# Optimization experiments

Hardware: AMD Instinct MI355X
Metric: run time of the kernel (lower is better)

Reference implementation:

```python
import jax, jax.numpy as jnp
import numpy as np

CHEB_K = 3

def avwgcn(x, E, W_pool, b_pool):
    # x: [B,N,Cin], E: [N,e], W_pool: [e,K,Cin,Cout], b_pool: [e,Cout]
    N = E.shape[0]
    A = jax.nn.softmax(jax.nn.relu(E @ E.T), axis=1)          # adaptive adjacency [N,N]
    supports = [jnp.eye(N, dtype=x.dtype), A]
    for _ in range(2, CHEB_K):
        supports.append(2.0 * (A @ supports[-1]) - supports[-2])
    S = jnp.stack(supports)                                    # [K,N,N]
    W = jnp.einsum('ne,ekio->nkio', E, W_pool)                 # per-node weights
    b = E @ b_pool                                             # [N,Cout]
    xg = jnp.einsum('knm,bmi->bnki', S, x)                     # Chebyshev graph conv
    return jnp.einsum('bnki,nkio->bno', xg, W) + b


def setup_inputs() -> dict:
    key = jax.random.key(0)
    ks = jax.random.split(key, 7)
    B, N, Din, Dout, E_DIM = 64, 1024, 64, 64, 16
    C = Din + Dout
    return {
        'x': jax.random.normal(ks[0], (B, N, Din), dtype=jnp.float32),
        'state': jax.random.normal(ks[1], (B, N, Dout), dtype=jnp.float32),
        'node_embeddings': jax.random.normal(ks[2], (N, E_DIM), dtype=jnp.float32),
        'gate_W_pool': jax.random.normal(ks[3], (E_DIM, CHEB_K, C, 2 * Dout), dtype=jnp.float32) * 0.1,
        'gate_b_pool': jax.random.normal(ks[4], (E_DIM, 2 * Dout), dtype=jnp.float32) * 0.1,
        'upd_W_pool': jax.random.normal(ks[5], (E_DIM, CHEB_K, C, Dout), dtype=jnp.float32) * 0.1,
        'upd_b_pool': jax.random.normal(ks[6], (E_DIM, Dout), dtype=jnp.float32) * 0.1,
    }


def reference(x, state, node_embeddings, gate_W_pool, gate_b_pool, upd_W_pool, upd_b_pool):
    hidden_dim = state.shape[-1]
    input_and_state = jnp.concatenate([x, state], axis=-1)
    z_r = jax.nn.sigmoid(avwgcn(input_and_state, node_embeddings, gate_W_pool, gate_b_pool))
    z, r = z_r[..., :hidden_dim], z_r[..., hidden_dim:]
    candidate = jnp.concatenate([x, z * state], axis=-1)
    hc = jnp.tanh(avwgcn(candidate, node_embeddings, upd_W_pool, upd_b_pool))
    return r * state + (1.0 - r) * hc
```

## Files before the change

kernel.cpp:

```cpp
#include <hip/hip_runtime.h>
#include <math.h>

#define N_NODES 1024
#define B_SZ 64
#define GNH 4096
#define KI 384
#define EDIM 16
#define WG_NODE 49152
#define WG_WAVE 12288
#define WU_NODE 24576
#define WU_WAVE 6144

typedef _Float16 half8_t __attribute__((ext_vector_type(8)));
typedef float f32x4 __attribute__((ext_vector_type(4)));

__device__ __forceinline__ unsigned short f2h(float f) {
    _Float16 h = (_Float16)f;
    return *(unsigned short*)&h;
}
__device__ __forceinline__ float h2f(unsigned short u) {
    _Float16 h = *(_Float16*)&u;
    return (float)h;
}
__device__ __forceinline__ float sigmoidf_(float v) {
    return 1.f / (1.f + __expf(-v));
}
__device__ __forceinline__ void load_lds16(const void* g, void* l) {
    __builtin_amdgcn_global_load_lds(
        (const __attribute__((address_space(1))) void*)g,
        (__attribute__((address_space(3))) void*)l, 16, 0, 0);
}

__global__ __launch_bounds__(256) void compute_A_kernel(
    const float* __restrict__ E, unsigned short* __restrict__ Ah) {
    __shared__ float red[256];
    const int tid = threadIdx.x;
    const int n = blockIdx.x;
    float en[EDIM];
#pragma unroll
    for (int e = 0; e < EDIM; ++e) en[e] = E[n * EDIM + e];
    float logit[4], lmax = -1e30f;
#pragma unroll
    for (int j = 0; j < 4; ++j) {
        const int m = tid + j * 256;
        float d = 0.f;
#pragma unroll
        for (int e = 0; e < EDIM; ++e) d += en[e] * E[m * EDIM + e];
        d = fmaxf(d, 0.f);
        logit[j] = d;
        lmax = fmaxf(lmax, d);
    }
    red[tid] = lmax;
    __syncthreads();
    for (int s = 128; s > 0; s >>= 1) {
        if (tid < s) red[tid] = fmaxf(red[tid], red[tid + s]);
        __syncthreads();
    }
    lmax = red[0];
    __syncthreads();
    float ex[4], lsum = 0.f;
#pragma unroll
    for (int j = 0; j < 4; ++j) {
        ex[j] = __expf(logit[j] - lmax);
        lsum += ex[j];
    }
    red[tid] = lsum;
    __syncthreads();
    for (int s = 128; s > 0; s >>= 1) {
        if (tid < s) red[tid] += red[tid + s];
        __syncthreads();
    }
    const float inv = 1.f / red[0];
#pragma unroll
    for (int j = 0; j < 4; ++j)
        Ah[n * N_NODES + tid + j * 256] = f2h(ex[j] * inv);
}

__global__ __launch_bounds__(256) void build_T0_all_kernel(
    const float* __restrict__ x, const float* __restrict__ state,
    unsigned short* __restrict__ TX0, unsigned short* __restrict__ TS0,
    unsigned short* __restrict__ TX0T, unsigned short* __restrict__ TS0T) {
    __shared__ unsigned short Lx[64 * 72];
    __shared__ unsigned short Lss[64 * 72];
    const int tid = threadIdx.x;
    const int n0 = blockIdx.x * 64;
    const int b = blockIdx.y;
#pragma unroll
    for (int t = 0; t < 16; ++t) {
        const int id = t * 256 + tid;
        const int nl = id >> 6;
        const int c = id & 63;
        const float xv = x[((size_t)b * N_NODES + n0 + nl) * 64 + c];
        const float sv = state[((size_t)b * N_NODES + n0 + nl) * 64 + c];
        const unsigned short xh = f2h(xv), sh = f2h(sv);
        TX0[(size_t)(n0 + nl) * GNH + b * 64 + c] = xh;
        TS0[(size_t)(n0 + nl) * GNH + b * 64 + c] = sh;
        Lx[c * 72 + nl] = xh;
        Lss[c * 72 + nl] = sh;
    }
    __syncthreads();
#pragma unroll
    for (int t = 0; t < 2; ++t) {
        const int id = t * 256 + tid;
        const int c = id >> 3;
        const int n8 = id & 7;
        uint4 xv = *(const uint4*)&Lx[c * 72 + n8 * 8];
        uint4 sv = *(const uint4*)&Lss[c * 72 + n8 * 8];
        *(uint4*)&TX0T[(size_t)(b * 64 + c) * N_NODES + n0 + n8 * 8] = xv;
        *(uint4*)&TS0T[(size_t)(b * 64 + c) * N_NODES + n0 + n8 * 8] = sv;
    }
}

__global__ __launch_bounds__(256) void transpose16_kernel(
    const unsigned short* __restrict__ src, unsigned short* __restrict__ dst,
    int W) {
    __shared__ unsigned short Ls[64 * 72];
    const int tid = threadIdx.x;
    const int r0 = blockIdx.x * 64;
    const int c0 = blockIdx.y * 64;
#pragma unroll
    for (int t = 0; t < 2; ++t) {
        const int id = t * 256 + tid;
        const int row = id >> 3;
        const int c8 = id & 7;
        uint4 v = *(const uint4*)&src[(size_t)(r0 + row) * W + c0 + c8 * 8];
        const unsigned short* vp = (const unsigned short*)&v;
#pragma unroll
        for (int j = 0; j < 8; ++j) Ls[(c8 * 8 + j) * 72 + row] = vp[j];
    }
    __syncthreads();
#pragma unroll
    for (int t = 0; t < 2; ++t) {
        const int id = t * 256 + tid;
        const int c = id >> 3;
        const int r8 = id & 7;
        uint4 v = *(const uint4*)&Ls[c * 72 + r8 * 8];
        *(uint4*)&dst[(size_t)(c0 + c) * N_NODES + r0 + r8 * 8] = v;
    }
}

__global__ __launch_bounds__(256) void gemm_s2_kernel(
    const unsigned short* __restrict__ Ah,
    const unsigned short* __restrict__ AhT, unsigned short* __restrict__ S2h) {
    __shared__ unsigned short As[64 * 64];
    __shared__ unsigned short Bs[64 * 64];
    const int tid = threadIdx.x;
    const int wave = tid >> 6;
    const int lane = tid & 63;
    const int l15 = lane & 15;
    const int quad = lane >> 4;
    const int n0 = blockIdx.x * 64;
    const int m0 = blockIdx.y * 64;
    const int wn = wave * 16;
    const int lr = lane >> 3;
    const int lsw = (lane & 7) ^ lr;

    f32x4 acc[4] = {};
    for (int k0 = 0; k0 < N_NODES; k0 += 64) {
#pragma unroll
        for (int i = 0; i < 2; ++i) {
            const int rbase = (wave * 2 + i) * 8;
            load_lds16(&Ah[(size_t)(n0 + rbase + lr) * N_NODES + k0 + lsw * 8],
                       &As[rbase * 64]);
            load_lds16(&AhT[(size_t)(m0 + rbase + lr) * N_NODES + k0 + lsw * 8],
                       &Bs[rbase * 64]);
        }
        __syncthreads();
#pragma unroll
        for (int ks = 0; ks < 2; ++ks) {
            const int slot = ((ks * 4 + quad) ^ (l15 & 7)) * 8;
            const half8_t b = *(const half8_t*)&Bs[(wn + l15) * 64 + slot];
#pragma unroll
            for (int mi = 0; mi < 4; ++mi) {
                const half8_t a = *(const half8_t*)&As[(mi * 16 + l15) * 64 + slot];
                acc[mi] =
                    __builtin_amdgcn_mfma_f32_16x16x32_f16(a, b, acc[mi], 0, 0, 0);
            }
        }
        __syncthreads();
    }
#pragma unroll
    for (int mi = 0; mi < 4; ++mi) {
#pragma unroll
        for (int r = 0; r < 4; ++r) {
            const int n_g = n0 + mi * 16 + quad * 4 + r;
            const int m_g = m0 + wn + l15;
            const float v = 2.f * acc[mi][r] - (n_g == m_g ? 1.f : 0.f);
            S2h[(size_t)n_g * N_NODES + m_g] = f2h(v);
        }
    }
}

template <int BM>
__global__ __launch_bounds__(512, 2) void gemm_graph8_kernel(
    const unsigned short* __restrict__ Ah,
    const unsigned short* __restrict__ S2h,
    const unsigned short* __restrict__ BTX,
    const unsigned short* __restrict__ BTS,
    unsigned short* __restrict__ T1X, unsigned short* __restrict__ T1S,
    unsigned short* __restrict__ T2X, unsigned short* __restrict__ T2S,
    int ysplit, int colsPerXcd) {
    constexpr int MFR = BM / 32;
    constexpr int ASLOT_H = BM * 32;
    constexpr int SLOT_H = ASLOT_H + 8192;
    constexpr int APASS = BM / 128;
    constexpr int MT = 2048 / BM;
    __shared__ unsigned short lds[4 * SLOT_H];

    const int tid = threadIdx.x;
    const int wave = tid >> 6;
    const int lane = tid & 63;
    const int l15 = lane & 15;
    const int quad = lane >> 4;
    const int wm = (wave >> 2) * (BM / 2);
    const int wn = (wave & 3) * 64;

    const int id = blockIdx.x;
    const int xcd = id & 7;
    const int j = id >> 3;
    const int mtile = j & (MT - 1);
    const int ytile = xcd * colsPerXcd + j / MT;
    const int mrow0 = mtile * BM;
    const bool isA = mrow0 < N_NODES;
    const unsigned short* Asrc =
        (isA ? Ah : S2h) + (size_t)(mrow0 & 1023) * N_NODES;
    const bool isX = ytile < ysplit;
    const int col0 = (isX ? ytile : ytile - ysplit) * 256;
    const unsigned short* Bsrc = (isX ? BTX : BTS) + (size_t)col0 * N_NODES;
    unsigned short* OUT = (isA ? (isX ? T1X : T1S) : (isX ? T2X : T2S)) +
                          (size_t)(mrow0 & 1023) * GNH + col0;

    int goff[2];
#pragma unroll
    for (int jp = 0; jp < 2; ++jp) {
        const int cell = jp * 512 + tid;
        const int prow = cell >> 3;
        const int q = (cell & 7) ^ (prow & 7);
        goff[jp] = (2 * prow + (q >> 2)) * N_NODES + (q & 3) * 8;
    }

    int offA[MFR], offB[4];
#pragma unroll
    for (int mi = 0; mi < MFR; ++mi) {
        const int prow = (wm >> 1) + mi * 8 + (l15 >> 1);
        const int s8 = ((l15 & 1) * 4 + quad) ^ (prow & 7);
        offA[mi] = prow * 64 + s8 * 8;
    }
#pragma unroll
    for (int ni = 0; ni < 4; ++ni) {
        const int pcol = (wn >> 1) + ni * 8 + (l15 >> 1);
        const int s8 = ((l15 & 1) * 4 + quad) ^ (pcol & 7);
        offB[ni] = ASLOT_H + pcol * 64 + s8 * 8;
    }

    f32x4 acc[MFR][4] = {};

    auto stageA = [&](int t) {
        const int sl = t & 3;
#pragma unroll
        for (int jp = 0; jp < APASS; ++jp)
            load_lds16(Asrc + (size_t)t * 32 + goff[jp],
                       &lds[sl * SLOT_H + jp * 4096 + wave * 512]);
    };
    auto stageB = [&](int t) {
        const int sl = t & 3;
#pragma unroll
        for (int jp = 0; jp < 2; ++jp)
            load_lds16(Bsrc + (size_t)t * 32 + goff[jp],
                       &lds[sl * SLOT_H + ASLOT_H + jp * 4096 + wave * 512]);
    };
    auto waitPipe = [&] {
        if constexpr (BM == 256)
            asm volatile("s_waitcnt vmcnt(8)" ::: "memory");
        else
            asm volatile("s_waitcnt vmcnt(6)" ::: "memory");
    };

    auto tileBody = [&](int t, bool tail) {
        const unsigned short* base = &lds[(t & 3) * SLOT_H];
        half8_t a[MFR], b[4];
#pragma unroll
        for (int mi = 0; mi < MFR; ++mi)
            a[mi] = *(const half8_t*)&base[offA[mi]];
#pragma unroll
        for (int ni = 0; ni < 4; ++ni)
            b[ni] = *(const half8_t*)&base[offB[ni]];
        if (!tail) {
            stageA(t + 3);
            stageB(t + 3);
        }
        __builtin_amdgcn_sched_barrier(0);
        asm volatile("s_waitcnt lgkmcnt(0)" ::: "memory");
        __builtin_amdgcn_sched_barrier(0);
        __builtin_amdgcn_s_setprio(1);
#pragma unroll
        for (int mi = 0; mi < MFR; ++mi)
#pragma unroll
            for (int ni = 0; ni < 4; ++ni)
                acc[mi][ni] = __builtin_amdgcn_mfma_f32_16x16x32_f16(
                    a[mi], b[ni], acc[mi][ni], 0, 0, 0);
        __builtin_amdgcn_s_setprio(0);
        __builtin_amdgcn_sched_barrier(0);
        if (!tail) {
            waitPipe();
        } else {
            asm volatile("s_waitcnt vmcnt(0)" ::: "memory");
        }
        __builtin_amdgcn_sched_barrier(0);
        __builtin_amdgcn_s_barrier();
    };

    stageA(0); stageB(0);
    stageA(1); stageB(1);
    stageA(2); stageB(2);
    waitPipe();
    __builtin_amdgcn_s_barrier();
    __builtin_amdgcn_sched_barrier(0);

#pragma unroll 4
    for (int t = 0; t < 28; ++t) tileBody(t, false);
    tileBody(28, false);
    tileBody(29, true);
    tileBody(30, true);
    tileBody(31, true);

    constexpr int NPASS = BM / 64;
#pragma unroll
    for (int p = 0; p < NPASS; ++p) {
        __syncthreads();
        const int whalf = (BM == 256) ? (p >> 1) : p;
        const int mi0 = (BM == 256) ? (p & 1) * 4 : 0;
        if ((wave >> 2) == whalf) {
#pragma unroll
            for (int mi = 0; mi < 4; ++mi)
#pragma unroll
                for (int ni = 0; ni < 4; ++ni)
#pragma unroll
                    for (int r = 0; r < 4; ++r) {
                        const int row = mi * 16 + quad * 4 + r;
                        const int col = wn + ni * 16 + l15;
                        lds[row * 264 + col] = f2h(acc[mi0 + mi][ni][r]);
                    }
        }
        __syncthreads();
#pragma unroll
        for (int i = 0; i < 4; ++i) {
            const int id2 = i * 512 + tid;
            const int row = id2 >> 5;
            const int c8 = id2 & 31;
            uint4 v = *(const uint4*)&lds[row * 264 + c8 * 8];
            *(uint4*)&OUT[(size_t)(p * 64 + row) * GNH + c8 * 8] = v;
        }
    }
}

__global__ __launch_bounds__(256) void dequant_gate_kernel(
    const float* __restrict__ Wp, const float* __restrict__ E,
    unsigned short* __restrict__ Wt) {
    __shared__ float En[32 * 16];
    const int tid = threadIdx.x;
    const int c8 = blockIdx.x * 256 + tid;
    const int n0 = blockIdx.y * 32;
    const int sub = c8 & 1;
    const int c = c8 >> 1;
    const int l15 = c & 15;
    const int quad = (c >> 4) & 3;
    const int half = (c >> 6) & 1;
    const int ks = (c >> 7) & 3;
    const int sq = c >> 9;
    const int s = sq % 3;
    const int w = sq / 3;
    const int k0 = s * 128 + (ks * 4 + quad) * 8 + sub * 4;
    const int o = w * 32 + half * 16 + l15;

#pragma unroll
    for (int t = 0; t < 2; ++t) {
        const int id = t * 256 + tid;
        En[id] = E[(n0 + (id >> 4)) * EDIM + (id & 15)];
    }
    __syncthreads();

    f32x4 wv[EDIM];
#pragma unroll
    for (int e = 0; e < EDIM; ++e) {
        f32x4 v;
#pragma unroll
        for (int j = 0; j < 4; ++j)
            v[j] = Wp[(size_t)(e * KI + k0 + j) * 128 + o];
        wv[e] = v;
    }

#pragma unroll 4
    for (int nl = 0; nl < 32; ++nl) {
        f32x4 a = {0.f, 0.f, 0.f, 0.f};
#pragma unroll
        for (int e = 0; e < EDIM; ++e) a += wv[e] * En[nl * EDIM + e];
        union { unsigned short u[4]; uint2 v; } pk;
#pragma unroll
        for (int j = 0; j < 4; ++j) pk.u[j] = f2h(a[j]);
        *(uint2*)&Wt[(size_t)(n0 + nl) * WG_NODE + (size_t)c8 * 4] = pk.v;
    }
}

__global__ __launch_bounds__(256) void dequant_upd_kernel(
    const float* __restrict__ Wp, const float* __restrict__ E,
    unsigned short* __restrict__ Wt) {
    __shared__ float En[32 * 16];
    const int tid = threadIdx.x;
    const int c8 = blockIdx.x * 256 + tid;
    const int n0 = blockIdx.y * 32;
    const int sub = c8 & 1;
    const int c = c8 >> 1;
    const int l15 = c & 15;
    const int quad = (c >> 4) & 3;
    const int ks = (c >> 6) & 3;
    const int sq = c >> 8;
    const int s = sq % 3;
    const int w = sq / 3;
    const int k0 = s * 128 + (ks * 4 + quad) * 8 + sub * 4;
    const int o = w * 16 + l15;

#pragma unroll
    for (int t = 0; t < 2; ++t) {
        const int id = t * 256 + tid;
        En[id] = E[(n0 + (id >> 4)) * EDIM + (id & 15)];
    }
    __syncthreads();

    f32x4 wv[EDIM];
#pragma unroll
    for (int e = 0; e < EDIM; ++e) {
        f32x4 v;
#pragma unroll
        for (int j = 0; j < 4; ++j)
            v[j] = Wp[(size_t)(e * KI + k0 + j) * 64 + o];
        wv[e] = v;
    }

#pragma unroll 4
    for (int nl = 0; nl < 32; ++nl) {
        f32x4 a = {0.f, 0.f, 0.f, 0.f};
#pragma unroll
        for (int e = 0; e < EDIM; ++e) a += wv[e] * En[nl * EDIM + e];
        union { unsigned short u[4]; uint2 v; } pk;
#pragma unroll
        for (int j = 0; j < 4; ++j) pk.u[j] = f2h(a[j]);
        *(uint2*)&Wt[(size_t)(n0 + nl) * WU_NODE + (size_t)c8 * 4] = pk.v;
    }
}

__global__ __launch_bounds__(256) void pernode_gate_kernel(
    const unsigned short* __restrict__ TX0,
    const unsigned short* __restrict__ TS0,
    const unsigned short* __restrict__ TX1,
    const unsigned short* __restrict__ TS1,
    const unsigned short* __restrict__ TX2,
    const unsigned short* __restrict__ TS2,
    const unsigned short* __restrict__ Wt, const float* __restrict__ E,
    const float* __restrict__ bp, const float* __restrict__ state,
    unsigned short* __restrict__ rbuf, unsigned short* __restrict__ cand) {
    __shared__ unsigned short XsX[64 * 64];
    __shared__ unsigned short XsS[64 * 64];
    const int n = blockIdx.x;
    const int tid = threadIdx.x;
    const int wave = tid >> 6;
    const int lane = tid & 63;
    const int l15 = lane & 15;
    const int quad = lane >> 4;
    const int wn = wave * 32;
    const int lr = lane >> 3;
    const int lsw = (lane & 7) ^ lr;

    float bias[2];
#pragma unroll
    for (int ni = 0; ni < 2; ++ni) {
        float bv = 0.f;
#pragma unroll
        for (int e = 0; e < EDIM; ++e)
            bv += E[n * EDIM + e] * bp[e * 128 + wn + ni * 16 + l15];
        bias[ni] = bv;
    }

    f32x4 acc[4][2] = {};

    const unsigned short* TXs[3] = {TX0, TX1, TX2};
    const unsigned short* TSs[3] = {TS0, TS1, TS2};
    const unsigned short* wbase =
        Wt + ((size_t)n * 4 + wave) * WG_WAVE + lane * 8;

    for (int s = 0; s < 3; ++s) {
        const unsigned short* xs = TXs[s] + (size_t)n * GNH;
        const unsigned short* ss = TSs[s] + (size_t)n * GNH;
#pragma unroll
        for (int i = 0; i < 2; ++i) {
            const int slab = wave * 2 + i;
            load_lds16(xs + (slab * 8 + lr) * 64 + lsw * 8, &XsX[slab * 512]);
            load_lds16(ss + (slab * 8 + lr) * 64 + lsw * 8, &XsS[slab * 512]);
        }
        __syncthreads();
#pragma unroll
        for (int ks = 0; ks < 4; ++ks) {
            const int kseg = ks * 4 + quad;
            half8_t b[2];
            b[0] = *(const half8_t*)&wbase[((s * 4 + ks) * 2 + 0) * 512];
            b[1] = *(const half8_t*)&wbase[((s * 4 + ks) * 2 + 1) * 512];
            const unsigned short* plane = (kseg < 8) ? XsX : XsS;
            const int aslot = ((kseg & 7) ^ (l15 & 7)) * 8;
#pragma unroll
            for (int mi = 0; mi < 4; ++mi) {
                const half8_t a =
                    *(const half8_t*)&plane[(mi * 16 + l15) * 64 + aslot];
#pragma unroll
                for (int ni = 0; ni < 2; ++ni)
                    acc[mi][ni] = __builtin_amdgcn_mfma_f32_16x16x32_f16(
                        a, b[ni], acc[mi][ni], 0, 0, 0);
            }
        }
        __syncthreads();
    }

#pragma unroll
    for (int mi = 0; mi < 4; ++mi) {
#pragma unroll
        for (int r = 0; r < 4; ++r) {
            const int b_g = mi * 16 + quad * 4 + r;
#pragma unroll
            for (int ni = 0; ni < 2; ++ni) {
                const int o_g = wn + ni * 16 + l15;
                const float v = sigmoidf_(acc[mi][ni][r] + bias[ni]);
                if (o_g < 64) {
                    const float sv =
                        state[((size_t)b_g * N_NODES + n) * 64 + o_g];
                    cand[(size_t)n * GNH + b_g * 64 + o_g] = f2h(v * sv);
                } else {
                    rbuf[((size_t)n * B_SZ + b_g) * 64 + (o_g - 64)] = f2h(v);
                }
            }
        }
    }
}

__global__ __launch_bounds__(256) void pernode_upd_kernel(
    const unsigned short* __restrict__ TX0,
    const unsigned short* __restrict__ CAND,
    const unsigned short* __restrict__ TX1,
    const unsigned short* __restrict__ TS1,
    const unsigned short* __restrict__ TX2,
    const unsigned short* __restrict__ TS2,
    const unsigned short* __restrict__ Wt, const float* __restrict__ E,
    const float* __restrict__ bp, const float* __restrict__ state,
    const unsigned short* __restrict__ rbuf, float* __restrict__ out) {
    __shared__ unsigned short XsX[64 * 64];
    __shared__ unsigned short XsS[64 * 64];
    const int n = blockIdx.x;
    const int tid = threadIdx.x;
    const int wave = tid >> 6;
    const int lane = tid & 63;
    const int l15 = lane & 15;
    const int quad = lane >> 4;
    const int wn = wave * 16;
    const int o_g = wn + l15;
    const int lr = lane >> 3;
    const int lsw = (lane & 7) ^ lr;

    float bias = 0.f;
#pragma unroll
    for (int e = 0; e < EDIM; ++e)
        bias += E[n * EDIM + e] * bp[e * 64 + o_g];

    f32x4 acc[4] = {};

    const unsigned short* TXs[3] = {TX0, TX1, TX2};
    const unsigned short* TSs[3] = {CAND, TS1, TS2};
    const unsigned short* wbase =
        Wt + ((size_t)n * 4 + wave) * WU_WAVE + lane * 8;

    for (int s = 0; s < 3; ++s) {
        const unsigned short* xs = TXs[s] + (size_t)n * GNH;
        const unsigned short* ss = TSs[s] + (size_t)n * GNH;
#pragma unroll
        for (int i = 0; i < 2; ++i) {
            const int slab = wave * 2 + i;
            load_lds16(xs + (slab * 8 + lr) * 64 + lsw * 8, &XsX[slab * 512]);
            load_lds16(ss + (slab * 8 + lr) * 64 + lsw * 8, &XsS[slab * 512]);
        }
        __syncthreads();
#pragma unroll
        for (int ks = 0; ks < 4; ++ks) {
            const int kseg = ks * 4 + quad;
            const half8_t b = *(const half8_t*)&wbase[(s * 4 + ks) * 512];
            const unsigned short* plane = (kseg < 8) ? XsX : XsS;
            const int aslot = ((kseg & 7) ^ (l15 & 7)) * 8;
#pragma unroll
            for (int mi = 0; mi < 4; ++mi) {
                const half8_t a =
                    *(const half8_t*)&plane[(mi * 16 + l15) * 64 + aslot];
                acc[mi] = __builtin_amdgcn_mfma_f32_16x16x32_f16(a, b, acc[mi],
                                                                 0, 0, 0);
            }
        }
        __syncthreads();
    }

#pragma unroll
    for (int mi = 0; mi < 4; ++mi) {
#pragma unroll
        for (int r = 0; r < 4; ++r) {
            const int b_g = mi * 16 + quad * 4 + r;
            const float hc = tanhf(acc[mi][r] + bias);
            const float rr = h2f(rbuf[((size_t)n * B_SZ + b_g) * 64 + o_g]);
            const float sv = state[((size_t)b_g * N_NODES + n) * 64 + o_g];
            out[((size_t)b_g * N_NODES + n) * 64 + o_g] =
                rr * sv + (1.f - rr) * hc;
        }
    }
}

extern "C" void kernel_launch(void* const* d_in, const int* in_sizes, int n_in,
                              void* d_out, int out_size, void* d_ws,
                              size_t ws_size, hipStream_t stream) {
    const float* x = (const float*)d_in[0];
    const float* state = (const float*)d_in[1];
    const float* E = (const float*)d_in[2];
    const float* gW = (const float*)d_in[3];
    const float* gb = (const float*)d_in[4];
    const float* uW = (const float*)d_in[5];
    const float* ub = (const float*)d_in[6];
    float* out = (float*)d_out;

    char* ws = (char*)d_ws;
    unsigned short* Ah = (unsigned short*)ws;
    unsigned short* AhT = (unsigned short*)(ws + 2097152);
    unsigned short* S2h = (unsigned short*)(ws + 4194304);
    unsigned short* TX0 = (unsigned short*)(ws + 6291456);
    unsigned short* TS0 = (unsigned short*)(ws + 14680064);
    unsigned short* TX0T = (unsigned short*)(ws + 23068672);
    unsigned short* TS0T = (unsigned short*)(ws + 31457280);
    unsigned short* TX1 = (unsigned short*)(ws + 39845888);
    unsigned short* TS1 = (unsigned short*)(ws + 48234496);
    unsigned short* TX2 = (unsigned short*)(ws + 56623104);
    unsigned short* TS2 = (unsigned short*)(ws + 65011712);
    unsigned short* Wt = (unsigned short*)(ws + 73400320);
    unsigned short* rbuf = (unsigned short*)(ws + 174063616);
    unsigned short* CAND = (unsigned short*)(ws + 182452224);

    compute_A_kernel<<<N_NODES, 256, 0, stream>>>(E, Ah);
    build_T0_all_kernel<<<dim3(16, 64), 256, 0, stream>>>(x, state, TX0, TS0,
                                                          TX0T, TS0T);
    transpose16_kernel<<<dim3(16, 16), 256, 0, stream>>>(Ah, AhT, N_NODES);
    gemm_s2_kernel<<<dim3(16, 16), 256, 0, stream>>>(Ah, AhT, S2h);

    gemm_graph8_kernel<256><<<256, 512, 0, stream>>>(
        Ah, S2h, TX0T, TS0T, TX1, TS1, TX2, TS2, 16, 4);
    dequant_gate_kernel<<<dim3(48, 32), 256, 0, stream>>>(gW, E, Wt);
    pernode_gate_kernel<<<N_NODES, 256, 0, stream>>>(
        TX0, TS0, TX1, TS1, TX2, TS2, Wt, E, gb, state, rbuf, CAND);
    transpose16_kernel<<<dim3(16, 64), 256, 0, stream>>>(CAND, TS0T, GNH);

    gemm_graph8_kernel<128><<<256, 512, 0, stream>>>(
        Ah, S2h, TX0T, TS0T, TX1, TS1, TX2, TS2, 0, 2);
    dequant_upd_kernel<<<dim3(24, 32), 256, 0, stream>>>(uW, E, Wt);
    pernode_upd_kernel<<<N_NODES, 256, 0, stream>>>(
        TX0, CAND, TX1, TS1, TX2, TS2, Wt, E, ub, state, rbuf, out);
}
```

Before: 276.1 us.

## Fuse adjacency, input conversion and weight generation into one prep launch

```diff
diff --git a/kernel.cpp b/kernel.cpp
--- a/kernel.cpp
+++ b/kernel.cpp
@@ -31,83 +31,169 @@
         (__attribute__((address_space(3))) void*)l, 16, 0, 0);
 }
 
-__global__ __launch_bounds__(256) void compute_A_kernel(
-    const float* __restrict__ E, unsigned short* __restrict__ Ah) {
-    __shared__ float red[256];
+__global__ __launch_bounds__(256) void fused_prep_kernel(
+    const float* __restrict__ x, const float* __restrict__ state,
+    const float* __restrict__ E, const float* __restrict__ gW,
+    const float* __restrict__ uW, unsigned short* __restrict__ Ah,
+    unsigned short* __restrict__ TX0, unsigned short* __restrict__ TS0,
+    unsigned short* __restrict__ TX0T, unsigned short* __restrict__ TS0T,
+    unsigned short* __restrict__ WtG, unsigned short* __restrict__ WtU) {
+    __shared__ __align__(16) unsigned short sh[64 * 72 * 2];
     const int tid = threadIdx.x;
-    const int n = blockIdx.x;
-    float en[EDIM];
-#pragma unroll
-    for (int e = 0; e < EDIM; ++e) en[e] = E[n * EDIM + e];
-    float logit[4], lmax = -1e30f;
-#pragma unroll
-    for (int j = 0; j < 4; ++j) {
-        const int m = tid + j * 256;
-        float d = 0.f;
-#pragma unroll
-        for (int e = 0; e < EDIM; ++e) d += en[e] * E[m * EDIM + e];
-        d = fmaxf(d, 0.f);
-        logit[j] = d;
-        lmax = fmaxf(lmax, d);
-    }
-    red[tid] = lmax;
-    __syncthreads();
-    for (int s = 128; s > 0; s >>= 1) {
-        if (tid < s) red[tid] = fmaxf(red[tid], red[tid + s]);
-        __syncthreads();
-    }
-    lmax = red[0];
-    __syncthreads();
-    float ex[4], lsum = 0.f;
-#pragma unroll
-    for (int j = 0; j < 4; ++j) {
-        ex[j] = __expf(logit[j] - lmax);
-        lsum += ex[j];
-    }
-    red[tid] = lsum;
-    __syncthreads();
-    for (int s = 128; s > 0; s >>= 1) {
-        if (tid < s) red[tid] += red[tid + s];
-        __syncthreads();
-    }
-    const float inv = 1.f / red[0];
-#pragma unroll
-    for (int j = 0; j < 4; ++j)
-        Ah[n * N_NODES + tid + j * 256] = f2h(ex[j] * inv);
-}
-
-__global__ __launch_bounds__(256) void build_T0_all_kernel(
-    const float* __restrict__ x, const float* __restrict__ state,
-    unsigned short* __restrict__ TX0, unsigned short* __restrict__ TS0,
-    unsigned short* __restrict__ TX0T, unsigned short* __restrict__ TS0T) {
-    __shared__ unsigned short Lx[64 * 72];
-    __shared__ unsigned short Lss[64 * 72];
-    const int tid = threadIdx.x;
-    const int n0 = blockIdx.x * 64;
-    const int b = blockIdx.y;
-#pragma unroll
-    for (int t = 0; t < 16; ++t) {
-        const int id = t * 256 + tid;
-        const int nl = id >> 6;
-        const int c = id & 63;
-        const float xv = x[((size_t)b * N_NODES + n0 + nl) * 64 + c];
-        const float sv = state[((size_t)b * N_NODES + n0 + nl) * 64 + c];
-        const unsigned short xh = f2h(xv), sh = f2h(sv);
-        TX0[(size_t)(n0 + nl) * GNH + b * 64 + c] = xh;
-        TS0[(size_t)(n0 + nl) * GNH + b * 64 + c] = sh;
-        Lx[c * 72 + nl] = xh;
-        Lss[c * 72 + nl] = sh;
-    }
-    __syncthreads();
-#pragma unroll
-    for (int t = 0; t < 2; ++t) {
-        const int id = t * 256 + tid;
-        const int c = id >> 3;
-        const int n8 = id & 7;
-        uint4 xv = *(const uint4*)&Lx[c * 72 + n8 * 8];
-        uint4 sv = *(const uint4*)&Lss[c * 72 + n8 * 8];
-        *(uint4*)&TX0T[(size_t)(b * 64 + c) * N_NODES + n0 + n8 * 8] = xv;
-        *(uint4*)&TS0T[(size_t)(b * 64 + c) * N_NODES + n0 + n8 * 8] = sv;
+    const int blk = blockIdx.x;
+
+    if (blk < 1024) {
+        float* red = (float*)sh;
+        const int n = blk;
+        float en[EDIM];
+#pragma unroll
+        for (int e = 0; e < EDIM; ++e) en[e] = E[n * EDIM + e];
+        float logit[4], lmax = -1e30f;
+#pragma unroll
+        for (int j = 0; j < 4; ++j) {
+            const int m = tid + j * 256;
+            float d = 0.f;
+#pragma unroll
+            for (int e = 0; e < EDIM; ++e) d += en[e] * E[m * EDIM + e];
+            d = fmaxf(d, 0.f);
+            logit[j] = d;
+            lmax = fmaxf(lmax, d);
+        }
+        red[tid] = lmax;
+        __syncthreads();
+        for (int s = 128; s > 0; s >>= 1) {
+            if (tid < s) red[tid] = fmaxf(red[tid], red[tid + s]);
+            __syncthreads();
+        }
+        lmax = red[0];
+        __syncthreads();
+        float ex[4], lsum = 0.f;
+#pragma unroll
+        for (int j = 0; j < 4; ++j) {
+            ex[j] = __expf(logit[j] - lmax);
+            lsum += ex[j];
+        }
+        red[tid] = lsum;
+        __syncthreads();
+        for (int s = 128; s > 0; s >>= 1) {
+            if (tid < s) red[tid] += red[tid + s];
+            __syncthreads();
+        }
+        const float inv = 1.f / red[0];
+#pragma unroll
+        for (int j = 0; j < 4; ++j)
+            Ah[n * N_NODES + tid + j * 256] = f2h(ex[j] * inv);
+    } else if (blk < 2048) {
+        unsigned short* Lx = sh;
+        unsigned short* Lss = sh + 64 * 72;
+        const int idx = blk - 1024;
+        const int n0 = (idx & 15) * 64;
+        const int b = idx >> 4;
+#pragma unroll
+        for (int t = 0; t < 16; ++t) {
+            const int id = t * 256 + tid;
+            const int nl = id >> 6;
+            const int c = id & 63;
+            const float xv = x[((size_t)b * N_NODES + n0 + nl) * 64 + c];
+            const float sv = state[((size_t)b * N_NODES + n0 + nl) * 64 + c];
+            const unsigned short xh = f2h(xv), shv = f2h(sv);
+            TX0[(size_t)(n0 + nl) * GNH + b * 64 + c] = xh;
+            TS0[(size_t)(n0 + nl) * GNH + b * 64 + c] = shv;
+            Lx[c * 72 + nl] = xh;
+            Lss[c * 72 + nl] = shv;
+        }
+        __syncthreads();
+#pragma unroll
+        for (int t = 0; t < 2; ++t) {
+            const int id = t * 256 + tid;
+            const int c = id >> 3;
+            const int n8 = id & 7;
+            uint4 xv = *(const uint4*)&Lx[c * 72 + n8 * 8];
+            uint4 sv = *(const uint4*)&Lss[c * 72 + n8 * 8];
+            *(uint4*)&TX0T[(size_t)(b * 64 + c) * N_NODES + n0 + n8 * 8] = xv;
+            *(uint4*)&TS0T[(size_t)(b * 64 + c) * N_NODES + n0 + n8 * 8] = sv;
+        }
+    } else if (blk < 3584) {
+        float* En = (float*)sh;
+        const int idx = blk - 2048;
+        const int c8 = (idx % 48) * 256 + tid;
+        const int n0 = (idx / 48) * 32;
+        const int sub = c8 & 1;
+        const int c = c8 >> 1;
+        const int l15 = c & 15;
+        const int quad = (c >> 4) & 3;
+        const int half = (c >> 6) & 1;
+        const int ks = (c >> 7) & 3;
+        const int sq = c >> 9;
+        const int s = sq % 3;
+        const int w = sq / 3;
+        const int k0 = s * 128 + (ks * 4 + quad) * 8 + sub * 4;
+        const int o = w * 32 + half * 16 + l15;
+#pragma unroll
+        for (int t = 0; t < 2; ++t) {
+            const int id = t * 256 + tid;
+            En[id] = E[(n0 + (id >> 4)) * EDIM + (id & 15)];
+        }
+        __syncthreads();
+        f32x4 wv[EDIM];
+#pragma unroll
+        for (int e = 0; e < EDIM; ++e) {
+            f32x4 v;
+#pragma unroll
+            for (int j = 0; j < 4; ++j)
+                v[j] = gW[(size_t)(e * KI + k0 + j) * 128 + o];
+            wv[e] = v;
+        }
+#pragma unroll 4
+        for (int nl = 0; nl < 32; ++nl) {
+            f32x4 a = {0.f, 0.f, 0.f, 0.f};
+#pragma unroll
+            for (int e = 0; e < EDIM; ++e) a += wv[e] * En[nl * EDIM + e];
+            union { unsigned short u[4]; uint2 v; } pk;
+#pragma unroll
+            for (int j = 0; j < 4; ++j) pk.u[j] = f2h(a[j]);
+            *(uint2*)&WtG[(size_t)(n0 + nl) * WG_NODE + (size_t)c8 * 4] = pk.v;
+        }
+    } else {
+        float* En = (float*)sh;
+        const int idx = blk - 3584;
+        const int c8 = (idx % 24) * 256 + tid;
+        const int n0 = (idx / 24) * 32;
+        const int sub = c8 & 1;
+        const int c = c8 >> 1;
+        const int l15 = c & 15;
+        const int quad = (c >> 4) & 3;
+        const int ks = (c >> 6) & 3;
+        const int sq = c >> 8;
+        const int s = sq % 3;
+        const int w = sq / 3;
+        const int k0 = s * 128 + (ks * 4 + quad) * 8 + sub * 4;
+        const int o = w * 16 + l15;
+#pragma unroll
+        for (int t = 0; t < 2; ++t) {
+            const int id = t * 256 + tid;
+            En[id] = E[(n0 + (id >> 4)) * EDIM + (id & 15)];
+        }
+        __syncthreads();
+        f32x4 wv[EDIM];
+#pragma unroll
+        for (int e = 0; e < EDIM; ++e) {
+            f32x4 v;
+#pragma unroll
+            for (int j = 0; j < 4; ++j)
+                v[j] = uW[(size_t)(e * KI + k0 + j) * 64 + o];
+            wv[e] = v;
+        }
+#pragma unroll 4
+        for (int nl = 0; nl < 32; ++nl) {
+            f32x4 a = {0.f, 0.f, 0.f, 0.f};
+#pragma unroll
+            for (int e = 0; e < EDIM; ++e) a += wv[e] * En[nl * EDIM + e];
+            union { unsigned short u[4]; uint2 v; } pk;
+#pragma unroll
+            for (int j = 0; j < 4; ++j) pk.u[j] = f2h(a[j]);
+            *(uint2*)&WtU[(size_t)(n0 + nl) * WU_NODE + (size_t)c8 * 4] = pk.v;
+        }
     }
 }
 
@@ -351,101 +437,6 @@
             uint4 v = *(const uint4*)&lds[row * 264 + c8 * 8];
             *(uint4*)&OUT[(size_t)(p * 64 + row) * GNH + c8 * 8] = v;
         }
-    }
-}
-
-__global__ __launch_bounds__(256) void dequant_gate_kernel(
-    const float* __restrict__ Wp, const float* __restrict__ E,
-    unsigned short* __restrict__ Wt) {
-    __shared__ float En[32 * 16];
-    const int tid = threadIdx.x;
-    const int c8 = blockIdx.x * 256 + tid;
-    const int n0 = blockIdx.y * 32;
-    const int sub = c8 & 1;
-    const int c = c8 >> 1;
-    const int l15 = c & 15;
-    const int quad = (c >> 4) & 3;
-    const int half = (c >> 6) & 1;
-    const int ks = (c >> 7) & 3;
-    const int sq = c >> 9;
-    const int s = sq % 3;
-    const int w = sq / 3;
-    const int k0 = s * 128 + (ks * 4 + quad) * 8 + sub * 4;
-    const int o = w * 32 + half * 16 + l15;
-
-#pragma unroll
-    for (int t = 0; t < 2; ++t) {
-        const int id = t * 256 + tid;
-        En[id] = E[(n0 + (id >> 4)) * EDIM + (id & 15)];
-    }
-    __syncthreads();
-
-    f32x4 wv[EDIM];
-#pragma unroll
-    for (int e = 0; e < EDIM; ++e) {
-        f32x4 v;
-#pragma unroll
-        for (int j = 0; j < 4; ++j)
-            v[j] = Wp[(size_t)(e * KI + k0 + j) * 128 + o];
-        wv[e] = v;
-    }
-
-#pragma unroll 4
-    for (int nl = 0; nl < 32; ++nl) {
-        f32x4 a = {0.f, 0.f, 0.f, 0.f};
-#pragma unroll
-        for (int e = 0; e < EDIM; ++e) a += wv[e] * En[nl * EDIM + e];
-        union { unsigned short u[4]; uint2 v; } pk;
-#pragma unroll
-        for (int j = 0; j < 4; ++j) pk.u[j] = f2h(a[j]);
-        *(uint2*)&Wt[(size_t)(n0 + nl) * WG_NODE + (size_t)c8 * 4] = pk.v;
-    }
-}
-
-__global__ __launch_bounds__(256) void dequant_upd_kernel(
-    const float* __restrict__ Wp, const float* __restrict__ E,
-    unsigned short* __restrict__ Wt) {
-    __shared__ float En[32 * 16];
-    const int tid = threadIdx.x;
-    const int c8 = blockIdx.x * 256 + tid;
-    const int n0 = blockIdx.y * 32;
-    const int sub = c8 & 1;
-    const int c = c8 >> 1;
-    const int l15 = c & 15;
-    const int quad = (c >> 4) & 3;
-    const int ks = (c >> 6) & 3;
-    const int sq = c >> 8;
-    const int s = sq % 3;
-    const int w = sq / 3;
-    const int k0 = s * 128 + (ks * 4 + quad) * 8 + sub * 4;
-    const int o = w * 16 + l15;
-
-#pragma unroll
-    for (int t = 0; t < 2; ++t) {
-        const int id = t * 256 + tid;
-        En[id] = E[(n0 + (id >> 4)) * EDIM + (id & 15)];
-    }
-    __syncthreads();
-
-    f32x4 wv[EDIM];
-#pragma unroll
-    for (int e = 0; e < EDIM; ++e) {
-        f32x4 v;
-#pragma unroll
-        for (int j = 0; j < 4; ++j)
-            v[j] = Wp[(size_t)(e * KI + k0 + j) * 64 + o];
-        wv[e] = v;
-    }
-
-#pragma unroll 4
-    for (int nl = 0; nl < 32; ++nl) {
-        f32x4 a = {0.f, 0.f, 0.f, 0.f};
-#pragma unroll
-        for (int e = 0; e < EDIM; ++e) a += wv[e] * En[nl * EDIM + e];
-        union { unsigned short u[4]; uint2 v; } pk;
-#pragma unroll
-        for (int j = 0; j < 4; ++j) pk.u[j] = f2h(a[j]);
-        *(uint2*)&Wt[(size_t)(n0 + nl) * WU_NODE + (size_t)c8 * 4] = pk.v;
     }
 }
 
@@ -640,26 +631,24 @@
     unsigned short* TS1 = (unsigned short*)(ws + 48234496);
     unsigned short* TX2 = (unsigned short*)(ws + 56623104);
     unsigned short* TS2 = (unsigned short*)(ws + 65011712);
-    unsigned short* Wt = (unsigned short*)(ws + 73400320);
+    unsigned short* WtG = (unsigned short*)(ws + 73400320);
     unsigned short* rbuf = (unsigned short*)(ws + 174063616);
     unsigned short* CAND = (unsigned short*)(ws + 182452224);
-
-    compute_A_kernel<<<N_NODES, 256, 0, stream>>>(E, Ah);
-    build_T0_all_kernel<<<dim3(16, 64), 256, 0, stream>>>(x, state, TX0, TS0,
-                                                          TX0T, TS0T);
+    unsigned short* WtU = (unsigned short*)(ws + 190840832);
+
+    fused_prep_kernel<<<4352, 256, 0, stream>>>(
+        x, state, E, gW, uW, Ah, TX0, TS0, TX0T, TS0T, WtG, WtU);
     transpose16_kernel<<<dim3(16, 16), 256, 0, stream>>>(Ah, AhT, N_NODES);
     gemm_s2_kernel<<<dim3(16, 16), 256, 0, stream>>>(Ah, AhT, S2h);
 
     gemm_graph8_kernel<256><<<256, 512, 0, stream>>>(
         Ah, S2h, TX0T, TS0T, TX1, TS1, TX2, TS2, 16, 4);
-    dequant_gate_kernel<<<dim3(48, 32), 256, 0, stream>>>(gW, E, Wt);
     pernode_gate_kernel<<<N_NODES, 256, 0, stream>>>(
-        TX0, TS0, TX1, TS1, TX2, TS2, Wt, E, gb, state, rbuf, CAND);
+        TX0, TS0, TX1, TS1, TX2, TS2, WtG, E, gb, state, rbuf, CAND);
     transpose16_kernel<<<dim3(16, 64), 256, 0, stream>>>(CAND, TS0T, GNH);
 
     gemm_graph8_kernel<128><<<256, 512, 0, stream>>>(
         Ah, S2h, TX0T, TS0T, TX1, TS1, TX2, TS2, 0, 2);
-    dequant_upd_kernel<<<dim3(24, 32), 256, 0, stream>>>(uW, E, Wt);
     pernode_upd_kernel<<<N_NODES, 256, 0, stream>>>(
-        TX0, CAND, TX1, TS1, TX2, TS2, Wt, E, ub, state, rbuf, out);
-}
+        TX0, CAND, TX1, TS1, TX2, TS2, WtU, E, ub, state, rbuf, out);
+}
```

Result: faster. 263.8 us, median of 2 (-4.5%).
